# Kernel tuning notes

Hardware: AMD Instinct MI355X
Metric: run time of the kernel (lower is better)

Reference implementation:

```python
import jax, jax.numpy as jnp
import numpy as np

BS, L, D = 1, 2048, 4096  # L = hidden_size (seq len after permute), D = feature channels (loop count)


def setup_inputs() -> dict:
    key = jax.random.key(0)
    k1, k2, k3 = jax.random.split(key, 3)
    tokens_to_embrace_bs = jax.random.normal(k1, (BS, L, D), dtype=jnp.float32)
    W_in = 0.02 * jax.random.normal(k2, (L, L), dtype=jnp.float32)      # linear_in weight [out,in]
    W_out = 0.02 * jax.random.normal(k3, (L, 2 * L), dtype=jnp.float32)  # linear_out weight [out,in]
    return {"tokens_to_embrace_bs": tokens_to_embrace_bs, "W_in": W_in, "W_out": W_out}


def reference(tokens_to_embrace_bs, W_in, W_out):
    # context: [bs, D, L] -- each of the D feature channels is a length-L query
    context = jnp.transpose(tokens_to_embrace_bs, (0, 2, 1))
    # Fused version of the per-channel Python loop: all D queries at once.
    Q = jnp.einsum('bdl,ml->bdm', context, W_in)        # linear_in on every query -> [bs,D,L]
    S = jnp.einsum('bql,bkl->bqk', Q, context)          # attention scores [bs,D,D]
    A = jax.nn.softmax(S, axis=-1)                      # attention weights
    mix = jnp.einsum('bqk,bkl->bql', A, context)        # [bs,D,L]
    comb = jnp.concatenate([mix, Q], axis=-1)           # [bs,D,2L]
    out = jnp.tanh(jnp.einsum('bdc,lc->bdl', comb, W_out))  # attention output per channel [bs,D,L]
    # accumulate over the D loop iterations -> [bs,1,L] (bs=1, so broadcast add is exact)
    scores = out.sum(axis=1, keepdims=True)
    scores = scores / scores.max()
    scores = jax.nn.softmax(scores, axis=-1)
    return scores.squeeze()  # [L]
```

## Files before the change

kernel.cpp:

```cpp
#include <hip/hip_runtime.h>
#include <hip/hip_bf16.h>
#include <math.h>


typedef __attribute__((ext_vector_type(8))) short short8;
typedef __attribute__((ext_vector_type(4))) float f32x4;

__device__ __forceinline__ unsigned short f2bf(float f) {
  unsigned u = __float_as_uint(f);
  return (unsigned short)((u + 0x7FFF + ((u >> 16) & 1)) >> 16);
}

typedef const __attribute__((address_space(1))) unsigned int* gas_t;
typedef __attribute__((address_space(3))) unsigned int* las_t;
__device__ __forceinline__ void dma16(const unsigned short* g, unsigned short* l)
{
  __builtin_amdgcn_global_load_lds((gas_t)(const void*)g, (las_t)(void*)l,
                                   16, 0, 0);
}

template<int CMODE, int NXBS>
__global__ __launch_bounds__(512, 2) void gemm_n128(
    const unsigned short* __restrict__ A, const unsigned short* __restrict__ B,
    void* __restrict__ Cv, float* __restrict__ colsum,
    int K, int lda, int ldb, int ldc)
{
  __shared__ unsigned short sm[3][384 * 64];
  const int t = threadIdx.x;
  const int lane = t & 63, wid = t >> 6;
  const int wr = wid >> 2;
  const int wc = wid & 3;
  const int lr = lane & 15, lq = lane >> 4;

  int bx, by;
  {
    int wg = blockIdx.x;
    int q = (int)gridDim.x >> 3;
    int wgid = (wg & 7) * q + (wg >> 3);
    by = wgid >> NXBS;
    bx = wgid & ((1 << NXBS) - 1);
  }
  const int i0 = by * 256, j0 = bx * 128;

  const int r_ = t >> 3;
  const int ss_ = ((t & 7) ^ (r_ & 7)) * 8;

  auto issue = [&](int buf, int c, int k0) {
    const unsigned short* M;
    int ld, r0;
    if (c < 4) { M = A; ld = lda; r0 = i0 + c * 64; }
    else       { M = B; ld = ldb; r0 = j0 + (c - 4) * 64; }
    unsigned short* lb = &sm[buf][c * 4096];
    dma16(M + (size_t)(r0 + r_) * ld + k0 + ss_, lb + wid * 512);
  };

  auto frag = [&](const unsigned short* mat, int row, int kh) -> short8 {
    int lb = row * 128 + kh * 64 + (lq << 4);
    int pb = lb ^ ((row & 7) << 4);
    return *(const short8*)((const char*)mat + pb);
  };

  f32x4 acc[8][2];
  #pragma unroll
  for (int a = 0; a < 8; a++)
    #pragma unroll
    for (int b = 0; b < 2; b++) acc[a][b] = (f32x4){0.f, 0.f, 0.f, 0.f};

  #pragma unroll
  for (int c = 0; c < 6; c++) issue(0, c, 0);
  #pragma unroll
  for (int c = 0; c < 6; c++) issue(1, c, 64);
  asm volatile("s_waitcnt vmcnt(6)" ::: "memory");
  __builtin_amdgcn_s_barrier();

  const int NT = K >> 6;
  int cur = 0;
  for (int kt = 0; kt < NT; kt++) {
    const unsigned short* As = sm[cur];
    const unsigned short* Bs = sm[cur] + 256 * 64;
    const int b2 = (cur + 2 >= 3) ? cur - 1 : cur + 2;
    const int kn = (kt + 2) << 6;
    const bool st = (kt + 2 < NT);

    short8 af[4][2], bfr[2][2];
    #pragma unroll
    for (int m = 0; m < 4; m++) {
      af[m][0] = frag(As, wr * 128 + m * 16 + lr, 0);
      af[m][1] = frag(As, wr * 128 + m * 16 + lr, 1);
    }
    #pragma unroll
    for (int n = 0; n < 2; n++) {
      bfr[n][0] = frag(Bs, wc * 32 + n * 16 + lr, 0);
      bfr[n][1] = frag(Bs, wc * 32 + n * 16 + lr, 1);
    }
    if (st) {
      issue(b2, 0, kn); issue(b2, 2, kn);
      issue(b2, 4, kn); issue(b2, 5, kn);
    }
    __builtin_amdgcn_s_setprio(1);
    #pragma unroll
    for (int m = 0; m < 4; m++)
      #pragma unroll
      for (int n = 0; n < 2; n++) {
        acc[m][n] = __builtin_amdgcn_mfma_f32_16x16x32_bf16(
            af[m][0], bfr[n][0], acc[m][n], 0, 0, 0);
        acc[m][n] = __builtin_amdgcn_mfma_f32_16x16x32_bf16(
            af[m][1], bfr[n][1], acc[m][n], 0, 0, 0);
      }
    __builtin_amdgcn_s_setprio(0);

    #pragma unroll
    for (int m = 0; m < 4; m++) {
      af[m][0] = frag(As, wr * 128 + (4 + m) * 16 + lr, 0);
      af[m][1] = frag(As, wr * 128 + (4 + m) * 16 + lr, 1);
    }
    if (st) { issue(b2, 1, kn); issue(b2, 3, kn); }
    __builtin_amdgcn_s_setprio(1);
    #pragma unroll
    for (int m = 0; m < 4; m++)
      #pragma unroll
      for (int n = 0; n < 2; n++) {
        acc[4 + m][n] = __builtin_amdgcn_mfma_f32_16x16x32_bf16(
            af[m][0], bfr[n][0], acc[4 + m][n], 0, 0, 0);
        acc[4 + m][n] = __builtin_amdgcn_mfma_f32_16x16x32_bf16(
            af[m][1], bfr[n][1], acc[4 + m][n], 0, 0, 0);
      }
    __builtin_amdgcn_s_setprio(0);

    if (kt + 1 < NT) {
      if (st) asm volatile("s_waitcnt vmcnt(6)" ::: "memory");
      else    asm volatile("s_waitcnt vmcnt(0)" ::: "memory");
      __builtin_amdgcn_s_barrier();
    }
    cur = (cur + 1 == 3) ? 0 : cur + 1;
  }

  if (CMODE == 2) {
    #pragma unroll
    for (int n = 0; n < 2; n++) {
      float s = 0.f;
      #pragma unroll
      for (int m = 0; m < 8; m++)
        #pragma unroll
        for (int r = 0; r < 4; r++) s += tanhf(acc[m][n][r]);
      s += __shfl_xor(s, 16);
      s += __shfl_xor(s, 32);
      if (lq == 0) atomicAdd(&colsum[j0 + wc * 32 + n * 16 + lr], s);
    }
  } else {
    #pragma unroll
    for (int m = 0; m < 8; m++)
      #pragma unroll
      for (int n = 0; n < 2; n++)
        #pragma unroll
        for (int r = 0; r < 4; r++) {
          int row = i0 + wr * 128 + m * 16 + lq * 4 + r;
          int col = j0 + wc * 32 + n * 16 + lr;
          if (CMODE == 0)
            ((float*)Cv)[(size_t)row * ldc + col] = acc[m][n][r];
          else
            ((unsigned short*)Cv)[(size_t)row * ldc + col] = f2bf(acc[m][n][r]);
        }
  }
}

template<int BF32, int CMODE>
__global__ __launch_bounds__(256) void mfma_gemm(
    const unsigned short* __restrict__ Abf, const void* __restrict__ Bv,
    void* __restrict__ Cv, float* __restrict__ colsum,
    int K, int lda, int ldb, int ldc)
{
  __shared__ unsigned short As[128 * 32];
  __shared__ unsigned short Bs[128 * 32];
  const int t = threadIdx.x;
  const int lane = t & 63, wid = t >> 6;
  const int wm = (wid >> 1) * 64, wn = (wid & 1) * 64;
  const int i0 = blockIdx.y * 128, j0 = blockIdx.x * 128;
  const int lr = lane & 15, lq = lane >> 4;

  f32x4 acc[4][4];
  #pragma unroll
  for (int a = 0; a < 4; a++)
    #pragma unroll
    for (int b = 0; b < 4; b++) acc[a][b] = (f32x4){0.f, 0.f, 0.f, 0.f};

  for (int k0 = 0; k0 < K; k0 += 32) {
    #pragma unroll
    for (int u = 0; u < 2; u++) {
      int vid = u * 256 + t;
      int row = vid >> 2, kq = (vid & 3) * 8;
      dma16(Abf + (size_t)(i0 + row) * lda + k0 + kq,
            &As[(u * 256 + wid * 64) * 8]);
    }
    if (BF32 == 0) {
      #pragma unroll
      for (int u = 0; u < 2; u++) {
        int vid = u * 256 + t;
        int row = vid >> 2, kq = (vid & 3) * 8;
        dma16((const unsigned short*)Bv + (size_t)(j0 + row) * ldb + k0 + kq,
              &Bs[(u * 256 + wid * 64) * 8]);
      }
    } else {
      #pragma unroll
      for (int u = 0; u < 2; u++) {
        int vid = u * 256 + t;
        int row = vid >> 2, kq = (vid & 3) * 8;
        const float* s = (const float*)Bv + (size_t)(j0 + row) * ldb + k0 + kq;
        float4 f0 = *(const float4*)s;
        float4 f1 = *(const float4*)(s + 4);
        union { unsigned short h[8]; int4 v; } pk;
        pk.h[0] = f2bf(f0.x); pk.h[1] = f2bf(f0.y);
        pk.h[2] = f2bf(f0.z); pk.h[3] = f2bf(f0.w);
        pk.h[4] = f2bf(f1.x); pk.h[5] = f2bf(f1.y);
        pk.h[6] = f2bf(f1.z); pk.h[7] = f2bf(f1.w);
        *(int4*)&Bs[(size_t)vid * 8] = pk.v;
      }
    }
    __syncthreads();

    short8 af[4], bfr[4];
    #pragma unroll
    for (int tm = 0; tm < 4; tm++)
      af[tm] = *(const short8*)&As[(wm + tm * 16 + lr) * 32 + lq * 8];
    #pragma unroll
    for (int tn = 0; tn < 4; tn++)
      bfr[tn] = *(const short8*)&Bs[(wn + tn * 16 + lr) * 32 + lq * 8];

    #pragma unroll
    for (int tm = 0; tm < 4; tm++)
      #pragma unroll
      for (int tn = 0; tn < 4; tn++)
        acc[tm][tn] = __builtin_amdgcn_mfma_f32_16x16x32_bf16(
            af[tm], bfr[tn], acc[tm][tn], 0, 0, 0);
    __syncthreads();
  }

  if (CMODE == 2) {
    #pragma unroll
    for (int tn = 0; tn < 4; tn++) {
      float s = 0.f;
      #pragma unroll
      for (int tm = 0; tm < 4; tm++)
        #pragma unroll
        for (int r = 0; r < 4; r++) s += tanhf(acc[tm][tn][r]);
      s += __shfl_xor(s, 16);
      s += __shfl_xor(s, 32);
      if (lq == 0) atomicAdd(&colsum[j0 + wn + tn * 16 + lr], s);
    }
  } else {
    #pragma unroll
    for (int tm = 0; tm < 4; tm++)
      #pragma unroll
      for (int tn = 0; tn < 4; tn++)
        #pragma unroll
        for (int r = 0; r < 4; r++) {
          int row = i0 + wm + tm * 16 + lq * 4 + r;
          int col = j0 + wn + tn * 16 + lr;
          if (CMODE == 0)
            ((float*)Cv)[(size_t)row * ldc + col] = acc[tm][tn][r];
          else
            ((unsigned short*)Cv)[(size_t)row * ldc + col] = f2bf(acc[tm][tn][r]);
        }
  }
}

__global__ __launch_bounds__(256) void transpose_cvt_bf16(
    const float* __restrict__ T, unsigned short* __restrict__ Tt,
    unsigned short* __restrict__ Tb)
{
  __shared__ float tile[64][65];
  const int tx = threadIdx.x & 63;
  const int ty = threadIdx.x >> 6;
  const int k0 = blockIdx.x * 64;
  const int l0 = blockIdx.y * 64;
  #pragma unroll
  for (int u = 0; u < 16; u++) {
    int row = ty * 16 + u;
    float v = T[(size_t)(l0 + row) * 4096 + k0 + tx];
    tile[row][tx] = v;
    Tb[(size_t)(l0 + row) * 4096 + k0 + tx] = f2bf(v);
  }
  __syncthreads();
  #pragma unroll
  for (int u = 0; u < 16; u++) {
    int row = ty * 16 + u;
    Tt[(size_t)(k0 + row) * 2048 + l0 + tx] = f2bf(tile[tx][row]);
  }
}

__global__ __launch_bounds__(256) void transpose_bf16(
    const float* __restrict__ T, unsigned short* __restrict__ Tt)
{
  __shared__ float tile[64][65];
  const int tx = threadIdx.x & 63;
  const int ty = threadIdx.x >> 6;
  const int k0 = blockIdx.x * 64;
  const int l0 = blockIdx.y * 64;
  #pragma unroll
  for (int u = 0; u < 16; u++) {
    int row = ty * 16 + u;
    tile[row][tx] = T[(size_t)(l0 + row) * 4096 + k0 + tx];
  }
  __syncthreads();
  #pragma unroll
  for (int u = 0; u < 16; u++) {
    int row = ty * 16 + u;
    Tt[(size_t)(k0 + row) * 2048 + l0 + tx] = f2bf(tile[tx][row]);
  }
}

__global__ __launch_bounds__(256) void cvt_bf16(
    const float* __restrict__ in, unsigned short* __restrict__ out, int n8)
{
  int i = blockIdx.x * 256 + threadIdx.x;
  if (i >= n8) return;
  float4 f0 = ((const float4*)in)[(size_t)i * 2];
  float4 f1 = ((const float4*)in)[(size_t)i * 2 + 1];
  union { unsigned short h[8]; int4 v; } pk;
  pk.h[0] = f2bf(f0.x); pk.h[1] = f2bf(f0.y);
  pk.h[2] = f2bf(f0.z); pk.h[3] = f2bf(f0.w);
  pk.h[4] = f2bf(f1.x); pk.h[5] = f2bf(f1.y);
  pk.h[6] = f2bf(f1.z); pk.h[7] = f2bf(f1.w);
  ((int4*)out)[i] = pk.v;
}

__global__ __launch_bounds__(256) void softmax_bf16(float* __restrict__ S)
{
  float* p = S + (size_t)blockIdx.x * 4096;
  const int tid = threadIdx.x;
  float4 v[4];
  #pragma unroll
  for (int u = 0; u < 4; u++) v[u] = ((const float4*)p)[tid * 4 + u];

  float m = -3.4e38f;
  #pragma unroll
  for (int u = 0; u < 4; u++)
    m = fmaxf(m, fmaxf(fmaxf(v[u].x, v[u].y), fmaxf(v[u].z, v[u].w)));
  #pragma unroll
  for (int off = 32; off > 0; off >>= 1) m = fmaxf(m, __shfl_down(m, off, 64));
  __shared__ float redm[4];
  if ((tid & 63) == 0) redm[tid >> 6] = m;
  __syncthreads();
  m = fmaxf(fmaxf(redm[0], redm[1]), fmaxf(redm[2], redm[3]));

  float s = 0.f;
  #pragma unroll
  for (int u = 0; u < 4; u++) {
    v[u].x = __expf(v[u].x - m); v[u].y = __expf(v[u].y - m);
    v[u].z = __expf(v[u].z - m); v[u].w = __expf(v[u].w - m);
    s += v[u].x + v[u].y + v[u].z + v[u].w;
  }
  #pragma unroll
  for (int off = 32; off > 0; off >>= 1) s += __shfl_down(s, off, 64);
  __shared__ float reds[4];
  if ((tid & 63) == 0) reds[tid >> 6] = s;
  __syncthreads();
  s = reds[0] + reds[1] + reds[2] + reds[3];
  const float inv = 1.f / s;

  unsigned short* a = (unsigned short*)p;
  #pragma unroll
  for (int h = 0; h < 2; h++) {
    union { unsigned short u[8]; int4 q; } pk;
    #pragma unroll
    for (int j = 0; j < 2; j++) {
      float4 w = v[h * 2 + j];
      pk.u[j * 4 + 0] = f2bf(w.x * inv); pk.u[j * 4 + 1] = f2bf(w.y * inv);
      pk.u[j * 4 + 2] = f2bf(w.z * inv); pk.u[j * 4 + 3] = f2bf(w.w * inv);
    }
    ((int4*)a)[tid * 2 + h] = pk.q;
  }
}

__global__ void zero_k(float* p, int n)
{
  int i = blockIdx.x * 256 + threadIdx.x;
  if (i < n) p[i] = 0.f;
}

__global__ __launch_bounds__(256) void finalize_k(const float* __restrict__ scores,
                                                  float* __restrict__ out)
{
  const int tid = threadIdx.x;
  float s[8];
  #pragma unroll
  for (int u = 0; u < 8; u++) s[u] = scores[tid + u * 256];

  __shared__ float red[4];

  float m = -3.4e38f;
  #pragma unroll
  for (int u = 0; u < 8; u++) m = fmaxf(m, s[u]);
  #pragma unroll
  for (int off = 32; off > 0; off >>= 1) m = fmaxf(m, __shfl_down(m, off, 64));
  if ((tid & 63) == 0) red[tid >> 6] = m;
  __syncthreads();
  m = fmaxf(fmaxf(red[0], red[1]), fmaxf(red[2], red[3]));
  __syncthreads();

  const float inv1 = 1.f / m;
  #pragma unroll
  for (int u = 0; u < 8; u++) s[u] *= inv1;

  float m2 = -3.4e38f;
  #pragma unroll
  for (int u = 0; u < 8; u++) m2 = fmaxf(m2, s[u]);
  #pragma unroll
  for (int off = 32; off > 0; off >>= 1) m2 = fmaxf(m2, __shfl_down(m2, off, 64));
  if ((tid & 63) == 0) red[tid >> 6] = m2;
  __syncthreads();
  m2 = fmaxf(fmaxf(red[0], red[1]), fmaxf(red[2], red[3]));
  __syncthreads();

  float sum = 0.f;
  #pragma unroll
  for (int u = 0; u < 8; u++) { s[u] = expf(s[u] - m2); sum += s[u]; }
  #pragma unroll
  for (int off = 32; off > 0; off >>= 1) sum += __shfl_down(sum, off, 64);
  if ((tid & 63) == 0) red[tid >> 6] = sum;
  __syncthreads();
  sum = red[0] + red[1] + red[2] + red[3];

  const float invs = 1.f / sum;
  #pragma unroll
  for (int u = 0; u < 8; u++)
    out[tid + u * 256] = s[u] * invs;
}

extern "C" void kernel_launch(void* const* d_in, const int* in_sizes, int n_in,
                              void* d_out, int out_size, void* d_ws, size_t ws_size,
                              hipStream_t stream)
{
  const float* T    = (const float*)d_in[0];
  const float* Win  = (const float*)d_in[1];
  const float* Wout = (const float*)d_in[2];
  float* out = (float*)d_out;

  const size_t FIX1 = 92274688ull + 16384;
  int R = 1024; bool pre = false;
  if      (ws_size >= FIX1 + (size_t)4096 * 16384) { pre = true; R = 4096; }
  else if (ws_size >= FIX1 + (size_t)2048 * 16384) { pre = true; R = 2048; }
  else if (ws_size >= FIX1 + (size_t)1024 * 16384) { pre = true; R = 1024; }

  unsigned short* Tt = (unsigned short*)d_ws;

  if (pre) {
    unsigned short* Tb    = Tt + (size_t)4096 * 2048;
    unsigned short* Winb  = Tb + (size_t)2048 * 4096;
    unsigned short* Woutb = Winb + (size_t)2048 * 2048;
    unsigned short* comb  = Woutb + (size_t)2048 * 4096;
    float* S      = (float*)(comb + (size_t)4096 * 4096);
    float* scores = S + (size_t)R * 4096;

    zero_k<<<8, 256, 0, stream>>>(scores, 2048);
    transpose_cvt_bf16<<<dim3(64, 32), 256, 0, stream>>>(T, Tt, Tb);
    cvt_bf16<<<2048, 256, 0, stream>>>(Win, Winb, 524288);
    cvt_bf16<<<4096, 256, 0, stream>>>(Wout, Woutb, 1048576);

    gemm_n128<1, 4><<<256, 512, 0, stream>>>(
        Tt, Winb, comb + 2048, nullptr, 2048, 2048, 2048, 4096);
    for (int c = 0; c < 4096 / R; c++) {
      const size_t d0 = (size_t)c * R;
      if (R == 4096) {
        gemm_n128<0, 5><<<512, 512, 0, stream>>>(
            comb + 2048, Tt, S, nullptr, 2048, 4096, 2048, 4096);
      } else {
        mfma_gemm<0, 0><<<dim3(32, R / 128), 256, 0, stream>>>(
            comb + d0 * 4096 + 2048, Tt, S, nullptr, 2048, 4096, 2048, 4096);
      }
      softmax_bf16<<<R, 256, 0, stream>>>(S);
      if (R == 4096) {
        gemm_n128<1, 4><<<256, 512, 0, stream>>>(
            (unsigned short*)S, Tb, comb, nullptr, 4096, 8192, 4096, 4096);
      } else {
        mfma_gemm<0, 1><<<dim3(16, R / 128), 256, 0, stream>>>(
            (unsigned short*)S, Tb, comb + d0 * 4096, nullptr, 4096, 8192, 4096, 4096);
      }
    }
    gemm_n128<2, 4><<<256, 512, 0, stream>>>(
        comb, Woutb, nullptr, scores, 4096, 4096, 4096, 4096);
    finalize_k<<<1, 256, 0, stream>>>(scores, out);
  } else {
    unsigned short* comb = Tt + (size_t)4096 * 2048;
    float* S      = (float*)(comb + (size_t)4096 * 4096);
    float* scores = S + (size_t)1024 * 4096;

    zero_k<<<8, 256, 0, stream>>>(scores, 2048);
    transpose_bf16<<<dim3(64, 32), 256, 0, stream>>>(T, Tt);

    mfma_gemm<1, 1><<<dim3(16, 32), 256, 0, stream>>>(
        Tt, Win, comb + 2048, nullptr, 2048, 2048, 2048, 4096);
    for (int c = 0; c < 4; c++) {
      const size_t d0 = (size_t)c * 1024;
      mfma_gemm<0, 0><<<dim3(32, 8), 256, 0, stream>>>(
          comb + d0 * 4096 + 2048, Tt, S, nullptr, 2048, 4096, 2048, 4096);
      softmax_bf16<<<1024, 256, 0, stream>>>(S);
      mfma_gemm<1, 1><<<dim3(16, 8), 256, 0, stream>>>(
          (unsigned short*)S, T, comb + d0 * 4096, nullptr, 4096, 8192, 4096, 4096);
    }
    mfma_gemm<1, 2><<<dim3(16, 32), 256, 0, stream>>>(
        comb, Wout, nullptr, scores, 4096, 4096, 4096, 4096);
    finalize_k<<<1, 256, 0, stream>>>(scores, out);
  }
}
```

Baseline: 371.2 us.

## Reshape gemm_n128 warp tiling to 4x2 and remap workgroup swizzle per XCD

The 8 warps of gemm_n128 move from a 2x4 layout (each 128x32) to a 4x2 layout (each 64x64). This balances A and B fragment loads per warp and cuts LDS reads per MFMA. The block-to-tile mapping is replaced with a hardcoded XCD-aware swizzle that groups neighbouring tiles per XCD for L2 reuse. The fused transpose+convert kernel is split into a separate transpose and a flat cvt_bf16, which adds one extra read of the input.

```diff
diff --git a/kernel.cpp b/kernel.cpp
--- a/kernel.cpp
+++ b/kernel.cpp
@@ -28,17 +28,16 @@
   __shared__ unsigned short sm[3][384 * 64];
   const int t = threadIdx.x;
   const int lane = t & 63, wid = t >> 6;
-  const int wr = wid >> 2;
-  const int wc = wid & 3;
+  const int wr = wid >> 1;
+  const int wc = wid & 1;
   const int lr = lane & 15, lq = lane >> 4;
 
   int bx, by;
   {
     int wg = blockIdx.x;
-    int q = (int)gridDim.x >> 3;
-    int wgid = (wg & 7) * q + (wg >> 3);
-    by = wgid >> NXBS;
-    bx = wgid & ((1 << NXBS) - 1);
+    int x = wg & 7, s = wg >> 3;
+    if (NXBS == 4) { by = (x & 3) * 4 + (s >> 3); bx = (x >> 2) * 8 + (s & 7); }
+    else           { by = (x & 3) * 4 + (s >> 4); bx = (x >> 2) * 16 + (s & 15); }
   }
   const int i0 = by * 256, j0 = bx * 128;
 
@@ -60,11 +59,11 @@
     return *(const short8*)((const char*)mat + pb);
   };
 
-  f32x4 acc[8][2];
-  #pragma unroll
-  for (int a = 0; a < 8; a++)
-    #pragma unroll
-    for (int b = 0; b < 2; b++) acc[a][b] = (f32x4){0.f, 0.f, 0.f, 0.f};
+  f32x4 acc[4][4];
+  #pragma unroll
+  for (int a = 0; a < 4; a++)
+    #pragma unroll
+    for (int b = 0; b < 4; b++) acc[a][b] = (f32x4){0.f, 0.f, 0.f, 0.f};
 
   #pragma unroll
   for (int c = 0; c < 6; c++) issue(0, c, 0);
@@ -82,16 +81,16 @@
     const int kn = (kt + 2) << 6;
     const bool st = (kt + 2 < NT);
 
-    short8 af[4][2], bfr[2][2];
-    #pragma unroll
-    for (int m = 0; m < 4; m++) {
-      af[m][0] = frag(As, wr * 128 + m * 16 + lr, 0);
-      af[m][1] = frag(As, wr * 128 + m * 16 + lr, 1);
-    }
-    #pragma unroll
-    for (int n = 0; n < 2; n++) {
-      bfr[n][0] = frag(Bs, wc * 32 + n * 16 + lr, 0);
-      bfr[n][1] = frag(Bs, wc * 32 + n * 16 + lr, 1);
+    short8 af[2][2], bfr[4][2];
+    #pragma unroll
+    for (int m = 0; m < 2; m++) {
+      af[m][0] = frag(As, wr * 64 + m * 16 + lr, 0);
+      af[m][1] = frag(As, wr * 64 + m * 16 + lr, 1);
+    }
+    #pragma unroll
+    for (int n = 0; n < 4; n++) {
+      bfr[n][0] = frag(Bs, wc * 64 + n * 16 + lr, 0);
+      bfr[n][1] = frag(Bs, wc * 64 + n * 16 + lr, 1);
     }
     if (st) {
       issue(b2, 0, kn); issue(b2, 2, kn);
@@ -99,9 +98,9 @@
     }
     __builtin_amdgcn_s_setprio(1);
     #pragma unroll
-    for (int m = 0; m < 4; m++)
-      #pragma unroll
-      for (int n = 0; n < 2; n++) {
+    for (int m = 0; m < 2; m++)
+      #pragma unroll
+      for (int n = 0; n < 4; n++) {
         acc[m][n] = __builtin_amdgcn_mfma_f32_16x16x32_bf16(
             af[m][0], bfr[n][0], acc[m][n], 0, 0, 0);
         acc[m][n] = __builtin_amdgcn_mfma_f32_16x16x32_bf16(
@@ -110,20 +109,20 @@
     __builtin_amdgcn_s_setprio(0);
 
     #pragma unroll
-    for (int m = 0; m < 4; m++) {
-      af[m][0] = frag(As, wr * 128 + (4 + m) * 16 + lr, 0);
-      af[m][1] = frag(As, wr * 128 + (4 + m) * 16 + lr, 1);
+    for (int m = 0; m < 2; m++) {
+      af[m][0] = frag(As, wr * 64 + (2 + m) * 16 + lr, 0);
+      af[m][1] = frag(As, wr * 64 + (2 + m) * 16 + lr, 1);
     }
     if (st) { issue(b2, 1, kn); issue(b2, 3, kn); }
     __builtin_amdgcn_s_setprio(1);
     #pragma unroll
-    for (int m = 0; m < 4; m++)
-      #pragma unroll
-      for (int n = 0; n < 2; n++) {
-        acc[4 + m][n] = __builtin_amdgcn_mfma_f32_16x16x32_bf16(
-            af[m][0], bfr[n][0], acc[4 + m][n], 0, 0, 0);
-        acc[4 + m][n] = __builtin_amdgcn_mfma_f32_16x16x32_bf16(
-            af[m][1], bfr[n][1], acc[4 + m][n], 0, 0, 0);
+    for (int m = 0; m < 2; m++)
+      #pragma unroll
+      for (int n = 0; n < 4; n++) {
+        acc[2 + m][n] = __builtin_amdgcn_mfma_f32_16x16x32_bf16(
+            af[m][0], bfr[n][0], acc[2 + m][n], 0, 0, 0);
+        acc[2 + m][n] = __builtin_amdgcn_mfma_f32_16x16x32_bf16(
+            af[m][1], bfr[n][1], acc[2 + m][n], 0, 0, 0);
       }
     __builtin_amdgcn_s_setprio(0);
 
@@ -137,25 +136,25 @@
 
   if (CMODE == 2) {
     #pragma unroll
-    for (int n = 0; n < 2; n++) {
+    for (int n = 0; n < 4; n++) {
       float s = 0.f;
       #pragma unroll
-      for (int m = 0; m < 8; m++)
+      for (int m = 0; m < 4; m++)
         #pragma unroll
         for (int r = 0; r < 4; r++) s += tanhf(acc[m][n][r]);
       s += __shfl_xor(s, 16);
       s += __shfl_xor(s, 32);
-      if (lq == 0) atomicAdd(&colsum[j0 + wc * 32 + n * 16 + lr], s);
+      if (lq == 0) atomicAdd(&colsum[j0 + wc * 64 + n * 16 + lr], s);
     }
   } else {
     #pragma unroll
-    for (int m = 0; m < 8; m++)
-      #pragma unroll
-      for (int n = 0; n < 2; n++)
+    for (int m = 0; m < 4; m++)
+      #pragma unroll
+      for (int n = 0; n < 4; n++)
         #pragma unroll
         for (int r = 0; r < 4; r++) {
-          int row = i0 + wr * 128 + m * 16 + lq * 4 + r;
-          int col = j0 + wc * 32 + n * 16 + lr;
+          int row = i0 + wr * 64 + m * 16 + lq * 4 + r;
+          int col = j0 + wc * 64 + n * 16 + lr;
           if (CMODE == 0)
             ((float*)Cv)[(size_t)row * ldc + col] = acc[m][n][r];
           else
@@ -264,30 +263,6 @@
   }
 }
 
-__global__ __launch_bounds__(256) void transpose_cvt_bf16(
-    const float* __restrict__ T, unsigned short* __restrict__ Tt,
-    unsigned short* __restrict__ Tb)
-{
-  __shared__ float tile[64][65];
-  const int tx = threadIdx.x & 63;
-  const int ty = threadIdx.x >> 6;
-  const int k0 = blockIdx.x * 64;
-  const int l0 = blockIdx.y * 64;
-  #pragma unroll
-  for (int u = 0; u < 16; u++) {
-    int row = ty * 16 + u;
-    float v = T[(size_t)(l0 + row) * 4096 + k0 + tx];
-    tile[row][tx] = v;
-    Tb[(size_t)(l0 + row) * 4096 + k0 + tx] = f2bf(v);
-  }
-  __syncthreads();
-  #pragma unroll
-  for (int u = 0; u < 16; u++) {
-    int row = ty * 16 + u;
-    Tt[(size_t)(k0 + row) * 2048 + l0 + tx] = f2bf(tile[tx][row]);
-  }
-}
-
 __global__ __launch_bounds__(256) void transpose_bf16(
     const float* __restrict__ T, unsigned short* __restrict__ Tt)
 {
@@ -453,7 +428,8 @@
     float* scores = S + (size_t)R * 4096;
 
     zero_k<<<8, 256, 0, stream>>>(scores, 2048);
-    transpose_cvt_bf16<<<dim3(64, 32), 256, 0, stream>>>(T, Tt, Tb);
+    transpose_bf16<<<dim3(64, 32), 256, 0, stream>>>(T, Tt);
+    cvt_bf16<<<4096, 256, 0, stream>>>(T, Tb, 1048576);
     cvt_bf16<<<2048, 256, 0, stream>>>(Win, Winb, 524288);
     cvt_bf16<<<4096, 256, 0, stream>>>(Wout, Woutb, 1048576);
 
```

After: 381.1 us. 1.03x slower.
